# Kernel tuning notes

Hardware: AMD Instinct MI355X
Metric: run time of the kernel (lower is better)

## Reference

```python
import jax, jax.numpy as jnp
import numpy as np

H, W, WIN = 16, 6, 3  # tile height/width, SSIM window
C1, C2 = 0.01 ** 2, 0.03 ** 2  # kornia ssim constants (max_val=1.0)


def _gauss_kernel3():
    # kornia get_gaussian_kernel2d((3,3),(1.5,1.5)), normalized
    c = jnp.arange(WIN, dtype=jnp.float32) - (WIN - 1) / 2.0
    g = jnp.exp(-(c ** 2) / (2.0 * 1.5 ** 2))
    g = g / g.sum()
    k2 = jnp.outer(g, g)
    return (k2 / k2.sum()).reshape(-1)  # (9,)


def _patches3(x):
    # x: (N,H,W) -> (N,H,W,9) 3x3 reflect-padded neighborhoods (kornia filter2d border 'reflect')
    xp = jnp.pad(x, ((0, 0), (1, 1), (1, 1)), mode='reflect')
    rows = [xp[:, i:i + H, j:j + W] for i in range(WIN) for j in range(WIN)]
    return jnp.stack(rows, axis=-1)


def setup_inputs() -> dict:
    key = jax.random.key(0)
    k1, k2 = jax.random.split(key)
    img_tensor = jax.random.uniform(k1, (1, 1, 1024, 768), dtype=jnp.float32)
    chars = jax.random.uniform(k2, (95, 1, 16, 6), dtype=jnp.float32)
    return {"img_tensor": img_tensor, "chars": chars}


def reference(img_tensor, chars):
    img_h, img_w = img_tensor.shape[-2], img_tensor.shape[-1]
    n_rows, n_cols = img_h // H, img_w // W
    # nn.Unfold(kernel=(H,W), stride=(H,W)): row-major tiles, each flattened (h,w)
    tiles = img_tensor[0, 0].reshape(n_rows, H, n_cols, W).transpose(0, 2, 1, 3)
    tiles = tiles.reshape(-1, H, W)              # (nt,H,W)
    refs = chars[:, 0]                           # (nr,H,W)

    kflat = _gauss_kernel3()                     # (9,)
    Tp = _patches3(tiles)                        # (nt,H,W,9)
    Rp = _patches3(refs)                         # (nr,H,W,9)

    # per-image windowed stats (computed ONCE per tile / per ref)
    mu_t = Tp @ kflat                            # (nt,H,W)
    mu_r = Rp @ kflat                            # (nr,H,W)
    ex2_t = (Tp ** 2) @ kflat
    ex2_r = (Rp ** 2) @ kflat
    sig_t = ex2_t - mu_t ** 2
    sig_r = ex2_r - mu_r ** 2

    # pairwise cross term E[t*r]: contract kernel over the 3x3 window axis
    exr = jnp.einsum('thwk,rhwk->trhw', Tp * kflat, Rp)  # (nt,nr,H,W)

    mt = mu_t[:, None]                           # (nt,1,H,W)
    mr = mu_r[None, :]                           # (1,nr,H,W)
    sig_tr = exr - mt * mr
    num = (2.0 * mt * mr + C1) * (2.0 * sig_tr + C2)
    den = (mt ** 2 + mr ** 2 + C1) * (sig_t[:, None] + sig_r[None, :] + C2)
    scores = (num / den).mean(axis=(2, 3))       # (nt,nr)

    dens_t = tiles.mean(axis=(1, 2))             # (nt,)
    dens_r = refs.mean(axis=(1, 2))              # (nr,)
    scores = scores - 3.0 * jnp.abs(dens_t[:, None] - dens_r[None, :])

    best_indices = jnp.argmax(scores, axis=1)
    return best_indices.reshape(-1, n_cols)
```

## Files before the change

kernel.cpp:

```cpp
#include <hip/hip_runtime.h>
#include <math.h>


static constexpr float kC1 = 1.0e-4f;
static constexpr float kC2 = 9.0e-4f;

struct KF { float k[9]; };

__device__ __forceinline__ int refl(int x, int n) {
  if (x < 0) return -x;
  if (x >= n) return 2 * n - 2 - x;
  return x;
}

__global__ __launch_bounds__(128) void refprep_kernel(
    const float* __restrict__ chars, float* __restrict__ refdata,
    float* __restrict__ densR, KF kf) {
  const int hw = blockIdx.x;
  const int r = threadIdx.x;
  if (r >= 96) return;
  const int h = hw / 6, w = hw % 6;
  if (r < 95) {
    const float* cb = chars + r * 96;
    float wrv[9];
    float mu = 0.f, ex2 = 0.f;
#pragma unroll
    for (int i = 0; i < 3; ++i) {
      const int hh = refl(h + i - 1, 16);
#pragma unroll
      for (int j = 0; j < 3; ++j) {
        const int ww = refl(w + j - 1, 6);
        const float p = cb[hh * 6 + ww];
        const float kv = kf.k[i * 3 + j];
        wrv[i * 3 + j] = kv * p;
        mu += kv * p;
        ex2 += kv * p * p;
      }
    }
    const float sig = ex2 - mu * mu;
#pragma unroll
    for (int k = 0; k < 9; ++k) refdata[(hw * 12 + k) * 96 + r] = wrv[k];
    refdata[(hw * 12 + 9) * 96 + r]  = mu;
    refdata[(hw * 12 + 10) * 96 + r] = mu * mu + kC1;
    refdata[(hw * 12 + 11) * 96 + r] = sig + kC2;
  } else {
#pragma unroll
    for (int k = 0; k < 9; ++k) refdata[(hw * 12 + k) * 96 + r] = 0.f;
    refdata[(hw * 12 + 9) * 96 + r]  = 0.f;
    refdata[(hw * 12 + 10) * 96 + r] = kC1;
    refdata[(hw * 12 + 11) * 96 + r] = kC2;
  }
  if (hw == 0) {
    if (r < 95) {
      float s = 0.f;
      for (int i = 0; i < 96; ++i) s += chars[r * 96 + i];
      densR[r] = s * (1.0f / 96.0f);
    } else {
      densR[r] = 0.f;
    }
  }
}

__device__ __forceinline__ void stage_px(const float* __restrict__ src,
                                         float* dst, int lane) {
  const uintptr_t gs = (uintptr_t)src;
  const uintptr_t ls = (uintptr_t)dst;
#define G_(off) ((const __attribute__((address_space(1))) void*)(gs + (off)))
#define L_(off) ((__attribute__((address_space(3))) void*)(uint32_t)(ls + (off)))
  __builtin_amdgcn_global_load_lds(G_(0    + lane * 16), L_(0),    16, 0, 0);
  __builtin_amdgcn_global_load_lds(G_(1024 + lane * 16), L_(1024), 16, 0, 0);
  __builtin_amdgcn_global_load_lds(G_(2048 + lane * 16), L_(2048), 16, 0, 0);
  __builtin_amdgcn_global_load_lds(G_(3072 + lane * 16), L_(3072), 16, 0, 0);
  __builtin_amdgcn_global_load_lds(G_(4096 + lane * 4),  L_(4096), 4, 0, 0);
  __builtin_amdgcn_global_load_lds(G_(4352 + lane * 4),  L_(4352), 4, 0, 0);
#undef G_
#undef L_
}

__global__ __launch_bounds__(512, 2) void ssim_main_kernel(
    const float* __restrict__ img, const float* __restrict__ refdata,
    const float* __restrict__ densR, int* __restrict__ out, KF kf) {
  __shared__ float smem[32256];
  __shared__ float densT[32];
  float* padT = smem;
  float* statT = smem + 4608;

  const int tid = threadIdx.x;
  const int w = tid >> 6;
  const int lane = tid & 63;
  const int tthr = lane >> 4;
  const int rthr = lane & 15;
  const int tl0 = tthr * 8;
  const int r0 = rthr * 6;
  const int blk = blockIdx.x;
  const int row0 = blk >> 2;
  const int c0 = (blk & 3) * 32;
  const int hwBase = w * 12;
  float* rbuf = smem + 13824 + w * 2304;

  stage_px(refdata + (size_t)hwBase * 1152, rbuf, lane);

  for (int idx = tid; idx < 4608; idx += 512) {
    const int c = idx >> 5, tl = idx & 31;
    const int ph = c >> 3, pw = c & 7;
    const int h = refl(ph - 1, 16), ww = refl(pw - 1, 6);
    padT[idx] = img[(row0 * 16 + h) * 768 + (c0 + tl) * 6 + ww];
  }
  __syncthreads();

  if (tid < 32) {
    float s = 0.f;
    for (int h = 0; h < 16; ++h)
      for (int ww = 0; ww < 6; ++ww)
        s += padT[((h + 1) * 8 + (ww + 1)) * 32 + tid];
    densT[tid] = s * (1.0f / 96.0f);
  }
  for (int idx = tid; idx < 3072; idx += 512) {
    const int hw = idx >> 5, tl = idx & 31;
    const int h = hw / 6, ww = hw % 6;
    float mu = 0.f, ex2 = 0.f;
#pragma unroll
    for (int i = 0; i < 3; ++i)
#pragma unroll
      for (int j = 0; j < 3; ++j) {
        const float p = padT[((h + i) * 8 + (ww + j)) * 32 + tl];
        const float kv = kf.k[i * 3 + j];
        mu += kv * p;
        ex2 += kv * p * p;
      }
    const float sig = ex2 - mu * mu;
    statT[(0 * 96 + hw) * 32 + tl] = 2.0f * mu;
    statT[(1 * 96 + hw) * 32 + tl] = mu * mu;
    statT[(2 * 96 + hw) * 32 + tl] = sig;
  }
  __syncthreads();

  float num[8][6], den[8][6];
#pragma unroll
  for (int i = 0; i < 8; ++i)
#pragma unroll
    for (int j = 0; j < 6; ++j) { num[i][j] = 0.f; den[i][j] = 1.f; }

#pragma unroll 1
  for (int it = 0; it < 12; ++it) {
    const int hw = hwBase + it;
    const float* buf = rbuf + (it & 1) * 1152;

    if (it < 11) {
      asm volatile("s_waitcnt lgkmcnt(0)" ::: "memory");
      stage_px(refdata + (size_t)(hw + 1) * 1152, rbuf + ((it + 1) & 1) * 1152, lane);
      asm volatile("s_waitcnt vmcnt(6)" ::: "memory");
    } else {
      asm volatile("s_waitcnt vmcnt(0)" ::: "memory");
    }

    const int h6 = hw / 6, w6 = hw - h6 * 6;
    const int pb = (h6 * 8 + w6) * 32 + tl0;

    float exr[8][6];
#pragma unroll
    for (int i = 0; i < 8; ++i)
#pragma unroll
      for (int j = 0; j < 6; ++j) exr[i][j] = 0.f;

#pragma unroll
    for (int ik = 0; ik < 3; ++ik)
#pragma unroll
      for (int jk = 0; jk < 3; ++jk) {
        const int kk = ik * 3 + jk;
        const float4 t0 = *(const float4*)&padT[pb + (ik * 8 + jk) * 32];
        const float4 t1 = *(const float4*)&padT[pb + (ik * 8 + jk) * 32 + 4];
        const float tp[8] = {t0.x, t0.y, t0.z, t0.w, t1.x, t1.y, t1.z, t1.w};
        float wr[6];
#pragma unroll
        for (int jj = 0; jj < 3; ++jj) {
          const float2 t = *(const float2*)&buf[kk * 96 + r0 + jj * 2];
          wr[jj * 2] = t.x; wr[jj * 2 + 1] = t.y;
        }
#pragma unroll
        for (int i = 0; i < 8; ++i)
#pragma unroll
          for (int j = 0; j < 6; ++j)
            exr[i][j] = fmaf(tp[i], wr[j], exr[i][j]);
      }

    float twomt[8], mt2[8], sigt[8];
    {
      const int sb0 = hw * 32 + tl0;
      float4 v;
      v = *(const float4*)&statT[sb0];            twomt[0]=v.x; twomt[1]=v.y; twomt[2]=v.z; twomt[3]=v.w;
      v = *(const float4*)&statT[sb0 + 4];        twomt[4]=v.x; twomt[5]=v.y; twomt[6]=v.z; twomt[7]=v.w;
      v = *(const float4*)&statT[3072 + sb0];     mt2[0]=v.x; mt2[1]=v.y; mt2[2]=v.z; mt2[3]=v.w;
      v = *(const float4*)&statT[3072 + sb0 + 4]; mt2[4]=v.x; mt2[5]=v.y; mt2[6]=v.z; mt2[7]=v.w;
      v = *(const float4*)&statT[6144 + sb0];     sigt[0]=v.x; sigt[1]=v.y; sigt[2]=v.z; sigt[3]=v.w;
      v = *(const float4*)&statT[6144 + sb0 + 4]; sigt[4]=v.x; sigt[5]=v.y; sigt[6]=v.z; sigt[7]=v.w;
    }
    float mr[6], m2c[6], sgc[6];
#pragma unroll
    for (int jj = 0; jj < 3; ++jj) {
      float2 t;
      t = *(const float2*)&buf[864 + r0 + jj * 2];  mr[jj*2] = t.x;  mr[jj*2+1] = t.y;
      t = *(const float2*)&buf[960 + r0 + jj * 2];  m2c[jj*2] = t.x; m2c[jj*2+1] = t.y;
      t = *(const float2*)&buf[1056 + r0 + jj * 2]; sgc[jj*2] = t.x; sgc[jj*2+1] = t.y;
    }

#pragma unroll
    for (int i = 0; i < 8; ++i)
#pragma unroll
      for (int j = 0; j < 6; ++j) {
        const float am = twomt[i] * mr[j];
        const float n1 = am + kC1;
        const float n2 = fmaf(exr[i][j], 2.0f, kC2) - am;
        const float d1 = mt2[i] + m2c[j];
        const float d2 = sigt[i] + sgc[j];
        const float nn = n1 * n2;
        const float dd = d1 * d2;
        num[i][j] = fmaf(nn, den[i][j], num[i][j] * dd);
        den[i][j] *= dd;
      }

    if (it == 3 || it == 7) {
#pragma unroll
      for (int i = 0; i < 8; ++i)
#pragma unroll
        for (int j = 0; j < 6; ++j) {
          const float s = __builtin_amdgcn_rcpf(den[i][j]);
          num[i][j] *= s;
          den[i][j] *= s;
        }
    }
  }

  __syncthreads();
  float* sbuf = smem;
#pragma unroll
  for (int i = 0; i < 8; ++i)
#pragma unroll
    for (int j = 0; j < 6; ++j)
      sbuf[(w * 32 + tl0 + i) * 97 + r0 + j] = num[i][j] / den[i][j];
  __syncthreads();

  {
    const int tile = tid >> 4, rt = tid & 15, rr = rt * 6;
    const float dt = densT[tile];
    float best = -1e30f; int bi = 0;
#pragma unroll
    for (int j = 0; j < 6; ++j) {
      const int r = rr + j;
      if (r < 95) {
        float s = 0.f;
#pragma unroll
        for (int g = 0; g < 8; ++g) s += sbuf[(g * 32 + tile) * 97 + r];
        s = s * (1.0f / 96.0f) - 3.0f * fabsf(dt - densR[r]);
        if (s > best) { best = s; bi = r; }
      }
    }
#pragma unroll
    for (int m = 8; m >= 1; m >>= 1) {
      const float ob = __shfl_xor(best, m, 64);
      const int oi = __shfl_xor(bi, m, 64);
      if (ob > best || (ob == best && oi < bi)) { best = ob; bi = oi; }
    }
    if (rt == 0) out[row0 * 128 + c0 + tile] = bi;
  }
}

extern "C" void kernel_launch(void* const* d_in, const int* in_sizes, int n_in,
                              void* d_out, int out_size, void* d_ws, size_t ws_size,
                              hipStream_t stream) {
  (void)in_sizes; (void)n_in; (void)out_size; (void)ws_size;
  const float* img = (const float*)d_in[0];
  const float* chars = (const float*)d_in[1];
  int* out = (int*)d_out;
  float* refdata = (float*)d_ws;
  float* densR = refdata + 96 * 12 * 96;

  KF kf;
  {
    float gg[3], s = 0.f;
    for (int i = 0; i < 3; ++i) {
      const float c = (float)i - 1.0f;
      gg[i] = expf(-(c * c) / (2.0f * 1.5f * 1.5f));
      s += gg[i];
    }
    float gn[3];
    for (int i = 0; i < 3; ++i) gn[i] = gg[i] / s;
    float k2[9]; float ks = 0.f;
    for (int i = 0; i < 3; ++i)
      for (int j = 0; j < 3; ++j) { k2[i * 3 + j] = gn[i] * gn[j]; ks += k2[i * 3 + j]; }
    for (int k = 0; k < 9; ++k) kf.k[k] = k2[k] / ks;
  }

  hipLaunchKernelGGL(refprep_kernel, dim3(96), dim3(128), 0, stream,
                     chars, refdata, densR, kf);
  hipLaunchKernelGGL(ssim_main_kernel, dim3(256), dim3(512), 0, stream,
                     img, refdata, densR, out, kf);
}
```

Baseline: 50.52 us.

## Split reference set across two blocks per tile group with combine pass

Each block now handles half of the references (48), doubling the grid to 512 blocks, and per-thread work drops to 4 tiles by 6 refs. The ref data layout becomes per-ref rows of 12 floats, with the factor of 2 folded into the weights and mean, and the C2 constant folded into the accumulator init. Shared memory shrinks and the launch bound rises to 4 blocks per CU to improve occupancy and load balance. A third small kernel merges the two halves' argmax, which adds a launch and a scratch round-trip.

```diff
diff --git a/kernel.cpp b/kernel.cpp
--- a/kernel.cpp
+++ b/kernel.cpp
@@ -19,11 +19,15 @@
   const int hw = blockIdx.x;
   const int r = threadIdx.x;
   if (r >= 96) return;
+  const int half = r / 48;
+  const int rloc = r - half * 48;
+  const int rp = rloc / 6 + 8 * (rloc % 6);
+  float* row = refdata + ((size_t)(hw * 2 + half) * 48 + rp) * 12;
   const int h = hw / 6, w = hw % 6;
   if (r < 95) {
     const float* cb = chars + r * 96;
+    float mu = 0.f, ex2 = 0.f;
     float wrv[9];
-    float mu = 0.f, ex2 = 0.f;
 #pragma unroll
     for (int i = 0; i < 3; ++i) {
       const int hh = refl(h + i - 1, 16);
@@ -32,23 +36,23 @@
         const int ww = refl(w + j - 1, 6);
         const float p = cb[hh * 6 + ww];
         const float kv = kf.k[i * 3 + j];
-        wrv[i * 3 + j] = kv * p;
+        wrv[i * 3 + j] = 2.0f * kv * p;
         mu += kv * p;
         ex2 += kv * p * p;
       }
     }
     const float sig = ex2 - mu * mu;
 #pragma unroll
-    for (int k = 0; k < 9; ++k) refdata[(hw * 12 + k) * 96 + r] = wrv[k];
-    refdata[(hw * 12 + 9) * 96 + r]  = mu;
-    refdata[(hw * 12 + 10) * 96 + r] = mu * mu + kC1;
-    refdata[(hw * 12 + 11) * 96 + r] = sig + kC2;
+    for (int k = 0; k < 9; ++k) row[k] = wrv[k];
+    row[9]  = 2.0f * mu;
+    row[10] = mu * mu + kC1;
+    row[11] = sig + kC2;
   } else {
 #pragma unroll
-    for (int k = 0; k < 9; ++k) refdata[(hw * 12 + k) * 96 + r] = 0.f;
-    refdata[(hw * 12 + 9) * 96 + r]  = 0.f;
-    refdata[(hw * 12 + 10) * 96 + r] = kC1;
-    refdata[(hw * 12 + 11) * 96 + r] = kC2;
+    for (int k = 0; k < 9; ++k) row[k] = 0.f;
+    row[9]  = 0.f;
+    row[10] = kC1;
+    row[11] = kC2;
   }
   if (hw == 0) {
     if (r < 95) {
@@ -69,18 +73,15 @@
 #define L_(off) ((__attribute__((address_space(3))) void*)(uint32_t)(ls + (off)))
   __builtin_amdgcn_global_load_lds(G_(0    + lane * 16), L_(0),    16, 0, 0);
   __builtin_amdgcn_global_load_lds(G_(1024 + lane * 16), L_(1024), 16, 0, 0);
-  __builtin_amdgcn_global_load_lds(G_(2048 + lane * 16), L_(2048), 16, 0, 0);
-  __builtin_amdgcn_global_load_lds(G_(3072 + lane * 16), L_(3072), 16, 0, 0);
-  __builtin_amdgcn_global_load_lds(G_(4096 + lane * 4),  L_(4096), 4, 0, 0);
-  __builtin_amdgcn_global_load_lds(G_(4352 + lane * 4),  L_(4352), 4, 0, 0);
+  __builtin_amdgcn_global_load_lds(G_(2048 + lane * 4),  L_(2048), 4, 0, 0);
 #undef G_
 #undef L_
 }
 
-__global__ __launch_bounds__(512, 2) void ssim_main_kernel(
+__global__ __launch_bounds__(512, 4) void ssim_main_kernel(
     const float* __restrict__ img, const float* __restrict__ refdata,
-    const float* __restrict__ densR, int* __restrict__ out, KF kf) {
-  __shared__ float smem[32256];
+    const float* __restrict__ densR, float2* __restrict__ scratch, KF kf) {
+  __shared__ float smem[19968];
   __shared__ float densT[32];
   float* padT = smem;
   float* statT = smem + 4608;
@@ -88,17 +89,18 @@
   const int tid = threadIdx.x;
   const int w = tid >> 6;
   const int lane = tid & 63;
-  const int tthr = lane >> 4;
-  const int rthr = lane & 15;
-  const int tl0 = tthr * 8;
-  const int r0 = rthr * 6;
+  const int tthr = lane >> 3;
+  const int rthr = lane & 7;
+  const int tl0 = tthr * 4;
   const int blk = blockIdx.x;
-  const int row0 = blk >> 2;
-  const int c0 = (blk & 3) * 32;
+  const int row0 = blk >> 3;
+  const int colg = (blk >> 1) & 3;
+  const int half = blk & 1;
+  const int c0 = colg * 32;
   const int hwBase = w * 12;
-  float* rbuf = smem + 13824 + w * 2304;
-
-  stage_px(refdata + (size_t)hwBase * 1152, rbuf, lane);
+  float* rbuf = smem + 10752 + w * 1152;
+
+  stage_px(refdata + (size_t)(hwBase * 2 + half) * 576, rbuf, lane);
 
   for (int idx = tid; idx < 4608; idx += 512) {
     const int c = idx >> 5, tl = idx & 31;
@@ -128,28 +130,27 @@
         mu += kv * p;
         ex2 += kv * p * p;
       }
-    const float sig = ex2 - mu * mu;
-    statT[(0 * 96 + hw) * 32 + tl] = 2.0f * mu;
-    statT[(1 * 96 + hw) * 32 + tl] = mu * mu;
-    statT[(2 * 96 + hw) * 32 + tl] = sig;
+    statT[idx] = mu;
+    statT[3072 + idx] = ex2 - mu * mu;
   }
   __syncthreads();
 
-  float num[8][6], den[8][6];
-#pragma unroll
-  for (int i = 0; i < 8; ++i)
+  float num[4][6], den[4][6];
+#pragma unroll
+  for (int i = 0; i < 4; ++i)
 #pragma unroll
     for (int j = 0; j < 6; ++j) { num[i][j] = 0.f; den[i][j] = 1.f; }
 
 #pragma unroll 1
   for (int it = 0; it < 12; ++it) {
     const int hw = hwBase + it;
-    const float* buf = rbuf + (it & 1) * 1152;
+    const float* buf = rbuf + (it & 1) * 576;
 
     if (it < 11) {
       asm volatile("s_waitcnt lgkmcnt(0)" ::: "memory");
-      stage_px(refdata + (size_t)(hw + 1) * 1152, rbuf + ((it + 1) & 1) * 1152, lane);
-      asm volatile("s_waitcnt vmcnt(6)" ::: "memory");
+      stage_px(refdata + (size_t)((hw + 1) * 2 + half) * 576,
+               rbuf + ((it + 1) & 1) * 576, lane);
+      asm volatile("s_waitcnt vmcnt(3)" ::: "memory");
     } else {
       asm volatile("s_waitcnt vmcnt(0)" ::: "memory");
     }
@@ -157,71 +158,81 @@
     const int h6 = hw / 6, w6 = hw - h6 * 6;
     const int pb = (h6 * 8 + w6) * 32 + tl0;
 
-    float exr[8][6];
-#pragma unroll
-    for (int i = 0; i < 8; ++i)
-#pragma unroll
-      for (int j = 0; j < 6; ++j) exr[i][j] = 0.f;
-
-#pragma unroll
-    for (int ik = 0; ik < 3; ++ik)
-#pragma unroll
-      for (int jk = 0; jk < 3; ++jk) {
-        const int kk = ik * 3 + jk;
-        const float4 t0 = *(const float4*)&padT[pb + (ik * 8 + jk) * 32];
-        const float4 t1 = *(const float4*)&padT[pb + (ik * 8 + jk) * 32 + 4];
-        const float tp[8] = {t0.x, t0.y, t0.z, t0.w, t1.x, t1.y, t1.z, t1.w};
-        float wr[6];
-#pragma unroll
-        for (int jj = 0; jj < 3; ++jj) {
-          const float2 t = *(const float2*)&buf[kk * 96 + r0 + jj * 2];
-          wr[jj * 2] = t.x; wr[jj * 2 + 1] = t.y;
-        }
-#pragma unroll
-        for (int i = 0; i < 8; ++i)
-#pragma unroll
-          for (int j = 0; j < 6; ++j)
-            exr[i][j] = fmaf(tp[i], wr[j], exr[i][j]);
-      }
-
-    float twomt[8], mt2[8], sigt[8];
+    float e[4][6];
+#pragma unroll
+    for (int i = 0; i < 4; ++i)
+#pragma unroll
+      for (int j = 0; j < 6; ++j) e[i][j] = kC2;
+
     {
-      const int sb0 = hw * 32 + tl0;
-      float4 v;
-      v = *(const float4*)&statT[sb0];            twomt[0]=v.x; twomt[1]=v.y; twomt[2]=v.z; twomt[3]=v.w;
-      v = *(const float4*)&statT[sb0 + 4];        twomt[4]=v.x; twomt[5]=v.y; twomt[6]=v.z; twomt[7]=v.w;
-      v = *(const float4*)&statT[3072 + sb0];     mt2[0]=v.x; mt2[1]=v.y; mt2[2]=v.z; mt2[3]=v.w;
-      v = *(const float4*)&statT[3072 + sb0 + 4]; mt2[4]=v.x; mt2[5]=v.y; mt2[6]=v.z; mt2[7]=v.w;
-      v = *(const float4*)&statT[6144 + sb0];     sigt[0]=v.x; sigt[1]=v.y; sigt[2]=v.z; sigt[3]=v.w;
-      v = *(const float4*)&statT[6144 + sb0 + 4]; sigt[4]=v.x; sigt[5]=v.y; sigt[6]=v.z; sigt[7]=v.w;
-    }
-    float mr[6], m2c[6], sgc[6];
-#pragma unroll
-    for (int jj = 0; jj < 3; ++jj) {
-      float2 t;
-      t = *(const float2*)&buf[864 + r0 + jj * 2];  mr[jj*2] = t.x;  mr[jj*2+1] = t.y;
-      t = *(const float2*)&buf[960 + r0 + jj * 2];  m2c[jj*2] = t.x; m2c[jj*2+1] = t.y;
-      t = *(const float2*)&buf[1056 + r0 + jj * 2]; sgc[jj*2] = t.x; sgc[jj*2+1] = t.y;
-    }
-
-#pragma unroll
-    for (int i = 0; i < 8; ++i)
+      float tpA[4][4];
+      {
+        const int off[4] = {0, 32, 64, 256};
+#pragma unroll
+        for (int k = 0; k < 4; ++k) {
+          const float4 t = *(const float4*)&padT[pb + off[k]];
+          tpA[k][0] = t.x; tpA[k][1] = t.y; tpA[k][2] = t.z; tpA[k][3] = t.w;
+        }
+      }
 #pragma unroll
       for (int j = 0; j < 6; ++j) {
-        const float am = twomt[i] * mr[j];
-        const float n1 = am + kC1;
-        const float n2 = fmaf(exr[i][j], 2.0f, kC2) - am;
-        const float d1 = mt2[i] + m2c[j];
-        const float d2 = sigt[i] + sgc[j];
-        const float nn = n1 * n2;
-        const float dd = d1 * d2;
-        num[i][j] = fmaf(nn, den[i][j], num[i][j] * dd);
-        den[i][j] *= dd;
-      }
+        const float4 wa = *(const float4*)&buf[(rthr + 8 * j) * 12];
+#pragma unroll
+        for (int i = 0; i < 4; ++i) {
+          e[i][j] = fmaf(tpA[0][i], wa.x, e[i][j]);
+          e[i][j] = fmaf(tpA[1][i], wa.y, e[i][j]);
+          e[i][j] = fmaf(tpA[2][i], wa.z, e[i][j]);
+          e[i][j] = fmaf(tpA[3][i], wa.w, e[i][j]);
+        }
+      }
+    }
+
+    float mu[4], sg[4];
+    {
+      const float4 m = *(const float4*)&statT[hw * 32 + tl0];
+      const float4 s = *(const float4*)&statT[3072 + hw * 32 + tl0];
+      mu[0]=m.x; mu[1]=m.y; mu[2]=m.z; mu[3]=m.w;
+      sg[0]=s.x; sg[1]=s.y; sg[2]=s.z; sg[3]=s.w;
+    }
+
+    {
+      float tpB[5][4];
+      {
+        const int off[5] = {288, 320, 512, 544, 576};
+#pragma unroll
+        for (int k = 0; k < 5; ++k) {
+          const float4 t = *(const float4*)&padT[pb + off[k]];
+          tpB[k][0] = t.x; tpB[k][1] = t.y; tpB[k][2] = t.z; tpB[k][3] = t.w;
+        }
+      }
+#pragma unroll
+      for (int j = 0; j < 6; ++j) {
+        const float4 wb = *(const float4*)&buf[(rthr + 8 * j) * 12 + 4];
+        const float4 wc = *(const float4*)&buf[(rthr + 8 * j) * 12 + 8];
+#pragma unroll
+        for (int i = 0; i < 4; ++i) {
+          float ev = e[i][j];
+          ev = fmaf(tpB[0][i], wb.x, ev);
+          ev = fmaf(tpB[1][i], wb.y, ev);
+          ev = fmaf(tpB[2][i], wb.z, ev);
+          ev = fmaf(tpB[3][i], wb.w, ev);
+          ev = fmaf(tpB[4][i], wc.x, ev);
+          const float am = mu[i] * wc.y;
+          const float n1 = am + kC1;
+          const float n2 = ev - am;
+          const float d1 = fmaf(mu[i], mu[i], wc.z);
+          const float d2 = sg[i] + wc.w;
+          const float nn = n1 * n2;
+          const float dd = d1 * d2;
+          num[i][j] = fmaf(nn, den[i][j], num[i][j] * dd);
+          den[i][j] *= dd;
+        }
+      }
+    }
 
     if (it == 3 || it == 7) {
 #pragma unroll
-      for (int i = 0; i < 8; ++i)
+      for (int i = 0; i < 4; ++i)
 #pragma unroll
         for (int j = 0; j < 6; ++j) {
           const float s = __builtin_amdgcn_rcpf(den[i][j]);
@@ -232,27 +243,28 @@
   }
 
   __syncthreads();
-  float* sbuf = smem;
-#pragma unroll
-  for (int i = 0; i < 8; ++i)
+  float* sb = smem;
+#pragma unroll
+  for (int i = 0; i < 4; ++i)
 #pragma unroll
     for (int j = 0; j < 6; ++j)
-      sbuf[(w * 32 + tl0 + i) * 97 + r0 + j] = num[i][j] / den[i][j];
+      sb[w * 1568 + (tl0 + i) * 49 + (rthr * 6 + j)] = num[i][j] / den[i][j];
   __syncthreads();
 
   {
-    const int tile = tid >> 4, rt = tid & 15, rr = rt * 6;
+    const int tile = tid >> 4, rt = tid & 15;
     const float dt = densT[tile];
     float best = -1e30f; int bi = 0;
 #pragma unroll
-    for (int j = 0; j < 6; ++j) {
-      const int r = rr + j;
-      if (r < 95) {
+    for (int q = 0; q < 3; ++q) {
+      const int rr = rt * 3 + q;
+      const int rg = half * 48 + rr;
+      if (rg < 95) {
         float s = 0.f;
 #pragma unroll
-        for (int g = 0; g < 8; ++g) s += sbuf[(g * 32 + tile) * 97 + r];
-        s = s * (1.0f / 96.0f) - 3.0f * fabsf(dt - densR[r]);
-        if (s > best) { best = s; bi = r; }
+        for (int g = 0; g < 8; ++g) s += sb[g * 1568 + tile * 49 + rr];
+        s = s * (1.0f / 96.0f) - 3.0f * fabsf(dt - densR[rg]);
+        if (s > best) { best = s; bi = rg; }
       }
     }
 #pragma unroll
@@ -261,8 +273,17 @@
       const int oi = __shfl_xor(bi, m, 64);
       if (ob > best || (ob == best && oi < bi)) { best = ob; bi = oi; }
     }
-    if (rt == 0) out[row0 * 128 + c0 + tile] = bi;
-  }
+    if (rt == 0)
+      scratch[half * 8192 + row0 * 128 + c0 + tile] = make_float2(best, (float)bi);
+  }
+}
+
+__global__ __launch_bounds__(256) void combine_kernel(
+    const float2* __restrict__ scratch, int* __restrict__ out) {
+  const int t = blockIdx.x * 256 + threadIdx.x;
+  const float2 a = scratch[t];
+  const float2 b = scratch[8192 + t];
+  out[t] = (b.x > a.x) ? (int)b.y : (int)a.y;
 }
 
 extern "C" void kernel_launch(void* const* d_in, const int* in_sizes, int n_in,
@@ -273,7 +294,8 @@
   const float* chars = (const float*)d_in[1];
   int* out = (int*)d_out;
   float* refdata = (float*)d_ws;
-  float* densR = refdata + 96 * 12 * 96;
+  float* densR = refdata + 110592;
+  float2* scratch = (float2*)(refdata + 110688);
 
   KF kf;
   {
@@ -293,6 +315,8 @@
 
   hipLaunchKernelGGL(refprep_kernel, dim3(96), dim3(128), 0, stream,
                      chars, refdata, densR, kf);
-  hipLaunchKernelGGL(ssim_main_kernel, dim3(256), dim3(512), 0, stream,
-                     img, refdata, densR, out, kf);
-}
+  hipLaunchKernelGGL(ssim_main_kernel, dim3(512), dim3(512), 0, stream,
+                     img, refdata, densR, scratch, kf);
+  hipLaunchKernelGGL(combine_kernel, dim3(32), dim3(256), 0, stream,
+                     scratch, out);
+}
```

After: 59.04 us. 16.9% more time.

## Store reference stats per-ref in AoS rows and accumulate SSIM with per-window reciprocal

Applied to the files above, without the earlier changes.

Reference data becomes one contiguous 12-float row per reference per pixel, permuted so each lane reads its refs with float4 loads. The factor of two is folded into the stored weights and mean, and the third tile-stat array is dropped. The running num/den product with periodic renormalisation is replaced by a direct per-window ratio, using a hardware reciprocal plus one Newton step, summed into a score accumulator. The aim is fewer LDS instructions and simpler accumulation, paid for with a reciprocal on every element. It also removes an LDS wait before the async prefetch and switches to incremental index arithmetic.

```diff
diff --git a/kernel.cpp b/kernel.cpp
--- a/kernel.cpp
+++ b/kernel.cpp
@@ -19,11 +19,13 @@
   const int hw = blockIdx.x;
   const int r = threadIdx.x;
   if (r >= 96) return;
+  const int rp = r / 6 + 16 * (r % 6);
+  float* row = refdata + ((size_t)hw * 96 + rp) * 12;
   const int h = hw / 6, w = hw % 6;
   if (r < 95) {
     const float* cb = chars + r * 96;
+    float mu = 0.f, ex2 = 0.f;
     float wrv[9];
-    float mu = 0.f, ex2 = 0.f;
 #pragma unroll
     for (int i = 0; i < 3; ++i) {
       const int hh = refl(h + i - 1, 16);
@@ -32,23 +34,23 @@
         const int ww = refl(w + j - 1, 6);
         const float p = cb[hh * 6 + ww];
         const float kv = kf.k[i * 3 + j];
-        wrv[i * 3 + j] = kv * p;
+        wrv[i * 3 + j] = 2.0f * kv * p;
         mu += kv * p;
         ex2 += kv * p * p;
       }
     }
     const float sig = ex2 - mu * mu;
 #pragma unroll
-    for (int k = 0; k < 9; ++k) refdata[(hw * 12 + k) * 96 + r] = wrv[k];
-    refdata[(hw * 12 + 9) * 96 + r]  = mu;
-    refdata[(hw * 12 + 10) * 96 + r] = mu * mu + kC1;
-    refdata[(hw * 12 + 11) * 96 + r] = sig + kC2;
+    for (int k = 0; k < 9; ++k) row[k] = wrv[k];
+    row[9]  = 2.0f * mu;
+    row[10] = mu * mu + kC1;
+    row[11] = sig + kC2;
   } else {
 #pragma unroll
-    for (int k = 0; k < 9; ++k) refdata[(hw * 12 + k) * 96 + r] = 0.f;
-    refdata[(hw * 12 + 9) * 96 + r]  = 0.f;
-    refdata[(hw * 12 + 10) * 96 + r] = kC1;
-    refdata[(hw * 12 + 11) * 96 + r] = kC2;
+    for (int k = 0; k < 9; ++k) row[k] = 0.f;
+    row[9]  = 0.f;
+    row[10] = kC1;
+    row[11] = kC2;
   }
   if (hw == 0) {
     if (r < 95) {
@@ -77,10 +79,11 @@
 #undef L_
 }
 
-__global__ __launch_bounds__(512, 2) void ssim_main_kernel(
+__global__ __launch_bounds__(512, 2)
+void ssim_main_kernel(
     const float* __restrict__ img, const float* __restrict__ refdata,
     const float* __restrict__ densR, int* __restrict__ out, KF kf) {
-  __shared__ float smem[32256];
+  __shared__ float smem[29184];
   __shared__ float densT[32];
   float* padT = smem;
   float* statT = smem + 4608;
@@ -91,12 +94,11 @@
   const int tthr = lane >> 4;
   const int rthr = lane & 15;
   const int tl0 = tthr * 8;
-  const int r0 = rthr * 6;
   const int blk = blockIdx.x;
   const int row0 = blk >> 2;
   const int c0 = (blk & 3) * 32;
   const int hwBase = w * 12;
-  float* rbuf = smem + 13824 + w * 2304;
+  float* rbuf = smem + 10752 + w * 2304;
 
   stage_px(refdata + (size_t)hwBase * 1152, rbuf, lane);
 
@@ -128,129 +130,112 @@
         mu += kv * p;
         ex2 += kv * p * p;
       }
-    const float sig = ex2 - mu * mu;
-    statT[(0 * 96 + hw) * 32 + tl] = 2.0f * mu;
-    statT[(1 * 96 + hw) * 32 + tl] = mu * mu;
-    statT[(2 * 96 + hw) * 32 + tl] = sig;
-  }
-  __syncthreads();
-
-  float num[8][6], den[8][6];
+    statT[idx] = mu;
+    statT[3072 + idx] = ex2 - mu * mu;
+  }
+  __syncthreads();
+
+  float score[8][6];
 #pragma unroll
   for (int i = 0; i < 8; ++i)
 #pragma unroll
-    for (int j = 0; j < 6; ++j) { num[i][j] = 0.f; den[i][j] = 1.f; }
+    for (int j = 0; j < 6; ++j) score[i][j] = 0.f;
+
+  int pb = (2 * w) * 8 * 32 + tl0;
+  int sbase = hwBase * 32 + tl0;
+  const float* refsrc = refdata + (size_t)(hwBase + 1) * 1152;
+  int w6 = 0;
 
 #pragma unroll 1
   for (int it = 0; it < 12; ++it) {
-    const int hw = hwBase + it;
     const float* buf = rbuf + (it & 1) * 1152;
 
     if (it < 11) {
-      asm volatile("s_waitcnt lgkmcnt(0)" ::: "memory");
-      stage_px(refdata + (size_t)(hw + 1) * 1152, rbuf + ((it + 1) & 1) * 1152, lane);
+      stage_px(refsrc, rbuf + ((it + 1) & 1) * 1152, lane);
       asm volatile("s_waitcnt vmcnt(6)" ::: "memory");
     } else {
       asm volatile("s_waitcnt vmcnt(0)" ::: "memory");
     }
-
-    const int h6 = hw / 6, w6 = hw - h6 * 6;
-    const int pb = (h6 * 8 + w6) * 32 + tl0;
-
-    float exr[8][6];
-#pragma unroll
-    for (int i = 0; i < 8; ++i)
-#pragma unroll
-      for (int j = 0; j < 6; ++j) exr[i][j] = 0.f;
-
+    refsrc += 1152;
+
+    float tp[9][8];
 #pragma unroll
     for (int ik = 0; ik < 3; ++ik)
 #pragma unroll
       for (int jk = 0; jk < 3; ++jk) {
-        const int kk = ik * 3 + jk;
-        const float4 t0 = *(const float4*)&padT[pb + (ik * 8 + jk) * 32];
-        const float4 t1 = *(const float4*)&padT[pb + (ik * 8 + jk) * 32 + 4];
-        const float tp[8] = {t0.x, t0.y, t0.z, t0.w, t1.x, t1.y, t1.z, t1.w};
-        float wr[6];
-#pragma unroll
-        for (int jj = 0; jj < 3; ++jj) {
-          const float2 t = *(const float2*)&buf[kk * 96 + r0 + jj * 2];
-          wr[jj * 2] = t.x; wr[jj * 2 + 1] = t.y;
-        }
-#pragma unroll
-        for (int i = 0; i < 8; ++i)
-#pragma unroll
-          for (int j = 0; j < 6; ++j)
-            exr[i][j] = fmaf(tp[i], wr[j], exr[i][j]);
-      }
-
-    float twomt[8], mt2[8], sigt[8];
+        const int k = ik * 3 + jk;
+        const float4 a = *(const float4*)&padT[pb + (ik * 8 + jk) * 32];
+        const float4 b = *(const float4*)&padT[pb + (ik * 8 + jk) * 32 + 4];
+        tp[k][0] = a.x; tp[k][1] = a.y; tp[k][2] = a.z; tp[k][3] = a.w;
+        tp[k][4] = b.x; tp[k][5] = b.y; tp[k][6] = b.z; tp[k][7] = b.w;
+      }
+
+    float mu[8], sg[8], mt2[8];
     {
-      const int sb0 = hw * 32 + tl0;
       float4 v;
-      v = *(const float4*)&statT[sb0];            twomt[0]=v.x; twomt[1]=v.y; twomt[2]=v.z; twomt[3]=v.w;
-      v = *(const float4*)&statT[sb0 + 4];        twomt[4]=v.x; twomt[5]=v.y; twomt[6]=v.z; twomt[7]=v.w;
-      v = *(const float4*)&statT[3072 + sb0];     mt2[0]=v.x; mt2[1]=v.y; mt2[2]=v.z; mt2[3]=v.w;
-      v = *(const float4*)&statT[3072 + sb0 + 4]; mt2[4]=v.x; mt2[5]=v.y; mt2[6]=v.z; mt2[7]=v.w;
-      v = *(const float4*)&statT[6144 + sb0];     sigt[0]=v.x; sigt[1]=v.y; sigt[2]=v.z; sigt[3]=v.w;
-      v = *(const float4*)&statT[6144 + sb0 + 4]; sigt[4]=v.x; sigt[5]=v.y; sigt[6]=v.z; sigt[7]=v.w;
-    }
-    float mr[6], m2c[6], sgc[6];
-#pragma unroll
-    for (int jj = 0; jj < 3; ++jj) {
-      float2 t;
-      t = *(const float2*)&buf[864 + r0 + jj * 2];  mr[jj*2] = t.x;  mr[jj*2+1] = t.y;
-      t = *(const float2*)&buf[960 + r0 + jj * 2];  m2c[jj*2] = t.x; m2c[jj*2+1] = t.y;
-      t = *(const float2*)&buf[1056 + r0 + jj * 2]; sgc[jj*2] = t.x; sgc[jj*2+1] = t.y;
-    }
-
-#pragma unroll
-    for (int i = 0; i < 8; ++i)
-#pragma unroll
-      for (int j = 0; j < 6; ++j) {
-        const float am = twomt[i] * mr[j];
+      v = *(const float4*)&statT[sbase];            mu[0]=v.x; mu[1]=v.y; mu[2]=v.z; mu[3]=v.w;
+      v = *(const float4*)&statT[sbase + 4];        mu[4]=v.x; mu[5]=v.y; mu[6]=v.z; mu[7]=v.w;
+      v = *(const float4*)&statT[3072 + sbase];     sg[0]=v.x; sg[1]=v.y; sg[2]=v.z; sg[3]=v.w;
+      v = *(const float4*)&statT[3072 + sbase + 4]; sg[4]=v.x; sg[5]=v.y; sg[6]=v.z; sg[7]=v.w;
+#pragma unroll
+      for (int i = 0; i < 8; ++i) mt2[i] = mu[i] * mu[i];
+    }
+
+#pragma unroll
+    for (int j = 0; j < 6; ++j) {
+      const int rb = (rthr + 16 * j) * 12;
+      const float4 wa = *(const float4*)&buf[rb];
+      const float4 wb = *(const float4*)&buf[rb + 4];
+      const float4 wc = *(const float4*)&buf[rb + 8];
+#pragma unroll
+      for (int i = 0; i < 8; ++i) {
+        float ev = fmaf(tp[0][i], wa.x, kC2);
+        ev = fmaf(tp[1][i], wa.y, ev);
+        ev = fmaf(tp[2][i], wa.z, ev);
+        ev = fmaf(tp[3][i], wa.w, ev);
+        ev = fmaf(tp[4][i], wb.x, ev);
+        ev = fmaf(tp[5][i], wb.y, ev);
+        ev = fmaf(tp[6][i], wb.z, ev);
+        ev = fmaf(tp[7][i], wb.w, ev);
+        ev = fmaf(tp[8][i], wc.x, ev);
+        const float am = mu[i] * wc.y;
         const float n1 = am + kC1;
-        const float n2 = fmaf(exr[i][j], 2.0f, kC2) - am;
-        const float d1 = mt2[i] + m2c[j];
-        const float d2 = sigt[i] + sgc[j];
+        const float n2 = ev - am;
+        const float d1 = mt2[i] + wc.z;
+        const float d2 = sg[i] + wc.w;
         const float nn = n1 * n2;
         const float dd = d1 * d2;
-        num[i][j] = fmaf(nn, den[i][j], num[i][j] * dd);
-        den[i][j] *= dd;
-      }
-
-    if (it == 3 || it == 7) {
-#pragma unroll
-      for (int i = 0; i < 8; ++i)
-#pragma unroll
-        for (int j = 0; j < 6; ++j) {
-          const float s = __builtin_amdgcn_rcpf(den[i][j]);
-          num[i][j] *= s;
-          den[i][j] *= s;
-        }
-    }
-  }
-
-  __syncthreads();
-  float* sbuf = smem;
+        const float r0v = __builtin_amdgcn_rcpf(dd);
+        const float r1v = r0v * fmaf(-dd, r0v, 2.0f);
+        score[i][j] = fmaf(nn, r1v, score[i][j]);
+      }
+    }
+
+    pb += (w6 == 5) ? 96 : 32;
+    w6 = (w6 == 5) ? 0 : w6 + 1;
+    sbase += 32;
+  }
+
+  __syncthreads();
+  float* sb = smem;
 #pragma unroll
   for (int i = 0; i < 8; ++i)
 #pragma unroll
     for (int j = 0; j < 6; ++j)
-      sbuf[(w * 32 + tl0 + i) * 97 + r0 + j] = num[i][j] / den[i][j];
+      sb[w * 3104 + (tl0 + i) * 97 + (rthr * 6 + j)] = score[i][j];
   __syncthreads();
 
   {
-    const int tile = tid >> 4, rt = tid & 15, rr = rt * 6;
+    const int tile = tid >> 4, rt = tid & 15;
     const float dt = densT[tile];
     float best = -1e30f; int bi = 0;
 #pragma unroll
-    for (int j = 0; j < 6; ++j) {
-      const int r = rr + j;
+    for (int q = 0; q < 6; ++q) {
+      const int r = rt * 6 + q;
       if (r < 95) {
         float s = 0.f;
 #pragma unroll
-        for (int g = 0; g < 8; ++g) s += sbuf[(g * 32 + tile) * 97 + r];
+        for (int g = 0; g < 8; ++g) s += sb[g * 3104 + tile * 97 + r];
         s = s * (1.0f / 96.0f) - 3.0f * fabsf(dt - densR[r]);
         if (s > best) { best = s; bi = r; }
       }
@@ -273,7 +258,7 @@
   const float* chars = (const float*)d_in[1];
   int* out = (int*)d_out;
   float* refdata = (float*)d_ws;
-  float* densR = refdata + 96 * 12 * 96;
+  float* densR = refdata + 110592;
 
   KF kf;
   {
```

New measurement: 50.38 us. No clear change (-0.3%).
